# Kernel tuning notes

Hardware: AMD Instinct MI355X
Metric: run time of the kernel (lower is better)

Reference implementation:

```python
import jax, jax.numpy as jnp
import numpy as np

B, S, N, D, H = 4, 2048, 2048, 1024, 16
HD = D // H  # 64
EPS = 1e-5


def layer_norm(x, w, b):
    m = x.mean(axis=-1, keepdims=True)
    v = ((x - m) ** 2).mean(axis=-1, keepdims=True)
    return (x - m) / jnp.sqrt(v + EPS) * w + b


def setup_inputs() -> dict:
    key = jax.random.key(0)
    ks = jax.random.split(key, 4)
    x_q = jax.random.normal(ks[0], (B, S, D), dtype=jnp.float32)
    x_k = jax.random.normal(ks[1], (B, N, HD), dtype=jnp.float32)
    x_v = jax.random.normal(ks[2], (B, N, HD), dtype=jnp.float32)
    # learned params
    qn_w = jnp.ones((HD,), jnp.float32)
    qn_b = jnp.zeros((HD,), jnp.float32)
    kn_w = jnp.ones((HD,), jnp.float32)
    kn_b = jnp.zeros((HD,), jnp.float32)
    n_w = jnp.ones((D,), jnp.float32)
    n_b = jnp.zeros((D,), jnp.float32)
    # xavier-uniform proj weight (D, D), no bias (proj_bias=False)
    limit = np.sqrt(6.0 / (D + D))
    proj_w = jax.random.uniform(ks[3], (D, D), jnp.float32, -limit, limit)
    return {"x_q": x_q, "x_k": x_k, "x_v": x_v,
            "qn_w": qn_w, "qn_b": qn_b, "kn_w": kn_w, "kn_b": kn_b,
            "n_w": n_w, "n_b": n_b, "proj_w": proj_w}


def reference(x_q, x_k, x_v, qn_w, qn_b, kn_w, kn_b, n_w, n_b, proj_w):
    scale = HD ** -0.5
    # faithful to torch: q.reshape(B, H, -1, head_dim) -- NO transpose before reshape
    q = x_q.reshape(B, H, S, HD)
    q = layer_norm(q, qn_w, qn_b)
    k = layer_norm(x_k, kn_w, kn_b)
    q = q * scale
    attn = jnp.einsum('bhsd,bnd->bhsn', q, k)  # (B,H,S,N) shared K across heads
    attn = jax.nn.softmax(attn, axis=-1)
    x = jnp.einsum('bhsn,bnd->bhsd', attn, x_v)  # shared V across heads
    x = jnp.transpose(x, (0, 2, 1, 3)).reshape(B, S, D)
    x = layer_norm(x, n_w, n_b)
    x = x @ proj_w.T  # nn.Linear: x W^T
    return x
```

## Files before the change

kernel.cpp:

```cpp
#include <hip/hip_runtime.h>

#define B_ 4
#define S_ 2048
#define N_ 2048
#define H_ 16
#define D_ 1024

typedef short s4v __attribute__((ext_vector_type(4)));
typedef short s8v __attribute__((ext_vector_type(8)));
typedef float f4v __attribute__((ext_vector_type(4)));
typedef float f2v __attribute__((ext_vector_type(2)));

__device__ __forceinline__ float bf2f(short s) {
  unsigned u = ((unsigned)(unsigned short)s) << 16;
  float f; __builtin_memcpy(&f, &u, 4); return f;
}
__device__ __forceinline__ short f2bf(float f) {
  unsigned u; __builtin_memcpy(&u, &f, 4);
  u += 0x7fffu + ((u >> 16) & 1u);
  return (short)(u >> 16);
}
__device__ __forceinline__ unsigned pack2bf(float a, float b) {
  unsigned ua, ub;
  __builtin_memcpy(&ua, &a, 4);
  __builtin_memcpy(&ub, &b, 4);
  return __builtin_amdgcn_perm(ub + 0x8000u, ua + 0x8000u, 0x07060302u);
}
__device__ __forceinline__ unsigned pk2(float a, float b) {
  unsigned ua, ub;
  __builtin_memcpy(&ua, &a, 4);
  __builtin_memcpy(&ub, &b, 4);
  return __builtin_amdgcn_perm(ub, ua, 0x07060302u);
}
__device__ __forceinline__ s8v load8f32(const float* p) {
  const f4v* q = (const f4v*)p;
  f4v a = q[0], b = q[1];
  union { s8v v; unsigned u[4]; } o;
  o.u[0] = pack2bf(a[0], a[1]); o.u[1] = pack2bf(a[2], a[3]);
  o.u[2] = pack2bf(b[0], b[1]); o.u[3] = pack2bf(b[2], b[3]);
  return o.v;
}
__device__ __forceinline__ void gld16(const char* g, char* l) {
  __builtin_amdgcn_global_load_lds(
      (const __attribute__((address_space(1))) unsigned*)g,
      (__attribute__((address_space(3))) unsigned*)l, 16, 0, 0);
}

__global__ __launch_bounds__(256) void prep_kernel(
    const float* __restrict__ xk, const float* __restrict__ knw,
    const float* __restrict__ knb, short* __restrict__ kws,
    const float* __restrict__ xv, short* __restrict__ vtp,
    const float* __restrict__ pw, const float* __restrict__ nw_,
    const float* __restrict__ nb_, short* __restrict__ wpb,
    float* __restrict__ t12) {
  __shared__ __align__(16) short vstage[4][2048];
  int blk = blockIdx.x;
  if (blk < 2048) {
    int gid = blk * 256 + threadIdx.x;
    int row = gid >> 6, lane = gid & 63;
    float v = xk[(size_t)row * 64 + lane];
    float s = v;
    #pragma unroll
    for (int mm = 1; mm < 64; mm <<= 1) s += __shfl_xor(s, mm, 64);
    float mean = s * 0.015625f;
    float d = v - mean;
    float vs = d * d;
    #pragma unroll
    for (int mm = 1; mm < 64; mm <<= 1) vs += __shfl_xor(vs, mm, 64);
    float rstd = rsqrtf(vs * 0.015625f + 1e-5f);
    kws[(size_t)row * 72 + lane] = f2bf(d * rstd * knw[lane] + knb[lane]);
  } else if (blk < 2112) {
    int wave = threadIdx.x >> 6, lane = threadIdx.x & 63;
    int u = (blk - 2048) * 4 + wave;
    int b = u >> 6, nb = u & 63;
    int r = lane >> 1, dh = lane & 1;
    const float* src = xv + ((size_t)(b * N_ + nb * 32 + r)) * 64 + dh * 32;
    int qq = (r & 15) >> 2;
    int slot = ((r >> 4) << 2) + (r & 3);
    short* wbase = &vstage[wave][0];
    #pragma unroll
    for (int jj = 0; jj < 32; jj += 4) {
      f4v f = *(const f4v*)(src + jj);
      #pragma unroll
      for (int e = 0; e < 4; e++) {
        int d = dh * 32 + jj + e;
        wbase[d * 32 + qq * 8 + slot] = f2bf(f[e]);
      }
    }
    __syncthreads();
    s8v* dst = (s8v*)(vtp + (size_t)u * 2560 + lane * 40);
    const s8v* sp = (const s8v*)(wbase + lane * 32);
    dst[0] = sp[0]; dst[1] = sp[1]; dst[2] = sp[2]; dst[3] = sp[3];
  } else {
    int jr = threadIdx.x >> 4;
    int lc = (threadIdx.x & 15) * 64;
    int j = (blk - 2112) * 16 + jr;
    const float* wr = pw + (size_t)j * 1024 + lc;
    float t1p = 0.f, t2p = 0.f;
    #pragma unroll
    for (int c = 0; c < 64; c += 8) {
      f4v w0 = *(const f4v*)(wr + c);
      f4v w1 = *(const f4v*)(wr + c + 4);
      f4v g0 = *(const f4v*)(nw_ + lc + c);
      f4v g1 = *(const f4v*)(nw_ + lc + c + 4);
      f4v b0 = *(const f4v*)(nb_ + lc + c);
      f4v b1 = *(const f4v*)(nb_ + lc + c + 4);
      float p[8];
      #pragma unroll
      for (int e = 0; e < 4; e++) {
        p[e]     = g0[e] * w0[e];
        p[4 + e] = g1[e] * w1[e];
        t1p += p[e] + p[4 + e];
        t2p += b0[e] * w0[e] + b1[e] * w1[e];
      }
      union { s8v v; unsigned u[4]; } o8;
      o8.u[0] = pack2bf(p[0], p[1]); o8.u[1] = pack2bf(p[2], p[3]);
      o8.u[2] = pack2bf(p[4], p[5]); o8.u[3] = pack2bf(p[6], p[7]);
      *(s8v*)(wpb + (size_t)j * 1024 + lc + c) = o8.v;
    }
    #pragma unroll
    for (int mm = 1; mm < 16; mm <<= 1) {
      t1p += __shfl_xor(t1p, mm, 64);
      t2p += __shfl_xor(t2p, mm, 64);
    }
    if ((threadIdx.x & 15) == 0) { t12[j * 2] = t1p; t12[j * 2 + 1] = t2p; }
  }
}

__global__ __launch_bounds__(256, 4) void flash_kernel(
    const float* __restrict__ xq, const float* __restrict__ qnw,
    const float* __restrict__ qnb, const short* __restrict__ kws,
    const short* __restrict__ vtp, short* __restrict__ aout) {
  __shared__ __align__(16) union {
    char qs[128 * 144];
    struct { char k[2][9216]; char v[2][10240]; } kv;
  } lds;
  int blk = blockIdx.x;
  int sblk = blk & 15, bh = blk >> 4, b = bh >> 4;
  int t = threadIdx.x, wave = t >> 6, lane = t & 63;
  int m = lane & 15, q = lane >> 4;
  const float QSCALE = 0.125f * 1.4426950408889634f;

  const char* kb = (const char*)kws + (size_t)b * N_ * 144;
  const char* vb = (const char*)vtp + (size_t)b * 64 * 5120;

  gld16(vb + t * 16,        lds.kv.v[0] + t * 16);
  gld16(vb + 4096 + t * 16, lds.kv.v[0] + 4096 + t * 16);
  if (t < 128) gld16(vb + 8192 + t * 16, lds.kv.v[0] + 8192 + t * 16);

  {
    int r = t >> 1, half = t & 1;
    const float* qr = xq + ((size_t)bh * S_ + sblk * 128 + r) * 64 + half * 32;
    f4v f[8];
    float s = 0.f, ss = 0.f;
    #pragma unroll
    for (int i = 0; i < 8; i++) {
      f[i] = *(const f4v*)(qr + i * 4);
      s += (f[i][0] + f[i][1]) + (f[i][2] + f[i][3]);
      ss += (f[i][0] * f[i][0] + f[i][1] * f[i][1]) + (f[i][2] * f[i][2] + f[i][3] * f[i][3]);
    }
    s += __shfl_xor(s, 1, 64);
    ss += __shfl_xor(ss, 1, 64);
    float mean = s * 0.015625f;
    float rstd = rsqrtf(ss * 0.015625f - mean * mean + 1e-5f);
    #pragma unroll
    for (int i = 0; i < 4; i++) {
      float y[8];
      #pragma unroll
      for (int e = 0; e < 4; e++) {
        int gi = half * 32 + i * 8;
        y[e]     = ((f[2 * i][e]     - mean) * rstd * qnw[gi + e]     + qnb[gi + e])     * QSCALE;
        y[4 + e] = ((f[2 * i + 1][e] - mean) * rstd * qnw[gi + 4 + e] + qnb[gi + 4 + e]) * QSCALE;
      }
      union { s8v v; unsigned u[4]; } o8;
      #pragma unroll
      for (int e = 0; e < 4; e++) o8.u[e] = pack2bf(y[2 * e], y[2 * e + 1]);
      *(s8v*)(lds.qs + r * 144 + half * 64 + i * 16) = o8.v;
    }
  }
  __syncthreads();

  s8v qlo[2], qhi[2];
  #pragma unroll
  for (int mt = 0; mt < 2; mt++) {
    const char* qrow = lds.qs + (wave * 32 + mt * 16 + m) * 144;
    qlo[mt] = *(const s8v*)(qrow + q * 16);
    qhi[mt] = *(const s8v*)(qrow + 64 + q * 16);
  }
  __syncthreads();

  gld16(kb + t * 16,        lds.kv.k[0] + t * 16);
  gld16(kb + 4096 + t * 16, lds.kv.k[0] + 4096 + t * 16);
  if (t < 64) gld16(kb + 8192 + t * 16, lds.kv.k[0] + 8192 + t * 16);
  __syncthreads();

  f4v zero4 = {0.f, 0.f, 0.f, 0.f};
  f4v o[2][4], lacc[2];
  #pragma unroll
  for (int mt = 0; mt < 2; mt++) {
    lacc[mt] = zero4;
    #pragma unroll
    for (int tt = 0; tt < 4; tt++) o[mt][tt] = zero4;
  }
  s8v ones;
  #pragma unroll
  for (int e = 0; e < 8; e++) ones[e] = (short)0x3F80;

  for (int it = 0; it < 32; ++it) {
    int cur = it & 1;
    if (it < 31) {
      const char* kg = kb + (size_t)(it + 1) * 9216;
      const char* vg = vb + (size_t)(it + 1) * 10240;
      char* kd = lds.kv.k[cur ^ 1];
      char* vd = lds.kv.v[cur ^ 1];
      gld16(kg + t * 16,        kd + t * 16);
      gld16(kg + 4096 + t * 16, kd + 4096 + t * 16);
      if (t < 64) gld16(kg + 8192 + t * 16, kd + 8192 + t * 16);
      gld16(vg + t * 16,        vd + t * 16);
      gld16(vg + 4096 + t * 16, vd + 4096 + t * 16);
      if (t < 128) gld16(vg + 8192 + t * 16, vd + 8192 + t * 16);
    }
    const char* kc = lds.kv.k[cur];
    const char* vc = lds.kv.v[cur];

    #pragma unroll
    for (int g = 0; g < 2; g++) {
      s8v a0lo = *(const s8v*)(kc + (g * 32 + m) * 144 + q * 16);
      s8v a0hi = *(const s8v*)(kc + (g * 32 + m) * 144 + 64 + q * 16);
      s8v a1lo = *(const s8v*)(kc + (g * 32 + 16 + m) * 144 + q * 16);
      s8v a1hi = *(const s8v*)(kc + (g * 32 + 16 + m) * 144 + 64 + q * 16);
      s8v vf[4];
      #pragma unroll
      for (int tt = 0; tt < 4; tt++)
        vf[tt] = *(const s8v*)(vc + g * 5120 + (tt * 16 + m) * 80 + q * 16);

      #pragma unroll
      for (int mt = 0; mt < 2; mt++) {
        f4v s0 = zero4, s1 = zero4;
        s0 = __builtin_amdgcn_mfma_f32_16x16x32_bf16(a0lo, qlo[mt], s0, 0, 0, 0);
        s0 = __builtin_amdgcn_mfma_f32_16x16x32_bf16(a0hi, qhi[mt], s0, 0, 0, 0);
        s1 = __builtin_amdgcn_mfma_f32_16x16x32_bf16(a1lo, qlo[mt], s1, 0, 0, 0);
        s1 = __builtin_amdgcn_mfma_f32_16x16x32_bf16(a1hi, qhi[mt], s1, 0, 0, 0);
        float p[8];
        #pragma unroll
        for (int i = 0; i < 4; i++) {
          p[i]     = __builtin_amdgcn_exp2f(s0[i]);
          p[4 + i] = __builtin_amdgcn_exp2f(s1[i]);
        }
        union { s8v v; unsigned u[4]; } pa;
        #pragma unroll
        for (int i = 0; i < 4; i++) pa.u[i] = pk2(p[2 * i], p[2 * i + 1]);
        lacc[mt] = __builtin_amdgcn_mfma_f32_16x16x32_bf16(pa.v, ones, lacc[mt], 0, 0, 0);
        #pragma unroll
        for (int tt = 0; tt < 4; tt++)
          o[mt][tt] = __builtin_amdgcn_mfma_f32_16x16x32_bf16(pa.v, vf[tt], o[mt][tt], 0, 0, 0);
      }
    }
    __syncthreads();
  }

  #pragma unroll
  for (int mt = 0; mt < 2; mt++) {
    #pragma unroll
    for (int i = 0; i < 4; i++) {
      float inv = __builtin_amdgcn_rcpf(lacc[mt][i]);
      int srow = sblk * 128 + wave * 32 + mt * 16 + q * 4 + i;
      size_t orow = ((size_t)b * S_ + srow) * D_ + (size_t)(bh & 15) * 64;
      #pragma unroll
      for (int tt = 0; tt < 4; tt++)
        aout[orow + tt * 16 + m] = f2bf(o[mt][tt][i] * inv);
    }
  }
}

__global__ __launch_bounds__(256) void ln_d_kernel(
    const short* __restrict__ x, const float* __restrict__ w,
    const float* __restrict__ bb, short* __restrict__ y) {
  int row = blockIdx.x * 4 + (threadIdx.x >> 6);
  int lane = threadIdx.x & 63;
  const short* xr = x + (size_t)row * D_ + lane * 16;
  s8v v0 = *(const s8v*)xr;
  s8v v1 = *(const s8v*)(xr + 8);
  float f[16];
  #pragma unroll
  for (int e = 0; e < 8; e++) { f[e] = bf2f(v0[e]); f[8 + e] = bf2f(v1[e]); }
  float s = 0.f, ss = 0.f;
  #pragma unroll
  for (int e = 0; e < 16; e++) { s += f[e]; ss += f[e] * f[e]; }
  #pragma unroll
  for (int mm = 1; mm < 64; mm <<= 1) {
    s += __shfl_xor(s, mm, 64);
    ss += __shfl_xor(ss, mm, 64);
  }
  float mean = s * (1.0f / 1024.0f);
  float rstd = rsqrtf(ss * (1.0f / 1024.0f) - mean * mean + 1e-5f);
  const float* wp = w + lane * 16;
  const float* bp = bb + lane * 16;
  union { s8v v[2]; short sh[16]; } o;
  #pragma unroll
  for (int e = 0; e < 16; e++)
    o.sh[e] = f2bf((f[e] - mean) * rstd * wp[e] + bp[e]);
  short* yr = y + (size_t)row * D_ + lane * 16;
  *(s8v*)yr = o.v[0];
  *(s8v*)(yr + 8) = o.v[1];
}

__global__ __launch_bounds__(256) void stats_kernel(
    const short* __restrict__ x, float* __restrict__ st) {
  int row = blockIdx.x * 4 + (threadIdx.x >> 6);
  int lane = threadIdx.x & 63;
  const short* xr = x + (size_t)row * D_ + lane * 16;
  s8v v0 = *(const s8v*)xr;
  s8v v1 = *(const s8v*)(xr + 8);
  float s = 0.f, ss = 0.f;
  #pragma unroll
  for (int e = 0; e < 8; e++) {
    float a = bf2f(v0[e]), b = bf2f(v1[e]);
    s += a + b; ss += a * a + b * b;
  }
  #pragma unroll
  for (int mm = 1; mm < 64; mm <<= 1) {
    s += __shfl_xor(s, mm, 64);
    ss += __shfl_xor(ss, mm, 64);
  }
  if (lane == 0) {
    float mean = s * (1.0f / 1024.0f);
    float rstd = rsqrtf(ss * (1.0f / 1024.0f) - mean * mean + 1e-5f);
    f2v o = {rstd, -mean * rstd};
    *(f2v*)(st + (size_t)row * 2) = o;
  }
}

__global__ __launch_bounds__(256, 2) void proj_gemm_fb(
    const short* __restrict__ A, const float* __restrict__ Bw,
    float* __restrict__ C) {
  __shared__ __align__(16) char la[2][16384];
  __shared__ __align__(16) char lb[2][16384];
  int wg = (blockIdx.x & 7) * 64 + (blockIdx.x >> 3);
  int bm = (wg >> 3) * 128;
  int bn = (wg & 7) * 128;
  int t = threadIdx.x, wave = t >> 6, lane = t & 63;
  int m = lane & 15, q = lane >> 4;
  int wm = (wave & 1) * 64, wn = (wave >> 1) * 64;

  int arow0 = t >> 3, au = t & 7;
  const char* abase = (const char*)(A + (size_t)bm * 1024);
  int brow = t >> 1, bu0 = (t & 1) * 4;
  const float* bwbase = Bw + (size_t)(bn + brow) * 1024;
  char* lbrow0 = lb[0] + brow * 128;
  char* lbrow1 = lb[1] + brow * 128;

  f4v zero4 = {0.f, 0.f, 0.f, 0.f};
  f4v acc[4][4];
  #pragma unroll
  for (int i = 0; i < 4; i++)
    #pragma unroll
    for (int j = 0; j < 4; j++) acc[i][j] = zero4;

  #pragma unroll
  for (int c = 0; c < 4; c++) {
    int row = c * 32 + arow0;
    gld16(abase + (size_t)row * 2048 + (size_t)(au ^ (row & 7)) * 16,
          la[0] + c * 4096 + t * 16);
  }
  #pragma unroll
  for (int j = 0; j < 4; j++) {
    int u = bu0 + j;
    s8v bv = load8f32(bwbase + u * 8);
    *(s8v*)(lbrow0 + ((u ^ (brow & 7)) * 16)) = bv;
  }
  __syncthreads();

  for (int it = 0; it < 16; ++it) {
    int cur = it & 1;
    if (it < 15) {
      int k0 = (it + 1) * 64;
      char* ad = la[cur ^ 1];
      char* bd = (cur ^ 1) ? lbrow1 : lbrow0;
      #pragma unroll
      for (int c = 0; c < 4; c++) {
        int row = c * 32 + arow0;
        gld16(abase + (size_t)row * 2048 + (size_t)k0 * 2 +
                  (size_t)(au ^ (row & 7)) * 16,
              ad + c * 4096 + t * 16);
      }
      #pragma unroll
      for (int j = 0; j < 4; j++) {
        int u = bu0 + j;
        s8v bv = load8f32(bwbase + k0 + u * 8);
        *(s8v*)(bd + ((u ^ (brow & 7)) * 16)) = bv;
      }
    }
    const char* lac = la[cur];
    const char* lbc = lb[cur];
    #pragma unroll
    for (int kh = 0; kh < 2; kh++) {
      s8v af[4], bfv[4];
      #pragma unroll
      for (int i = 0; i < 4; i++) {
        int r = wm + i * 16 + m;
        af[i] = *(const s8v*)(lac + r * 128 + (((kh * 4 + q) ^ (r & 7)) * 16));
      }
      #pragma unroll
      for (int j = 0; j < 4; j++) {
        int r = wn + j * 16 + m;
        bfv[j] = *(const s8v*)(lbc + r * 128 + (((kh * 4 + q) ^ (r & 7)) * 16));
      }
      #pragma unroll
      for (int i = 0; i < 4; i++)
        #pragma unroll
        for (int j = 0; j < 4; j++)
          acc[i][j] = __builtin_amdgcn_mfma_f32_16x16x32_bf16(af[i], bfv[j], acc[i][j], 0, 0, 0);
    }
    __syncthreads();
  }

  #pragma unroll
  for (int i = 0; i < 4; i++)
    #pragma unroll
    for (int j = 0; j < 4; j++)
      #pragma unroll
      for (int r = 0; r < 4; r++) {
        int row = bm + wm + i * 16 + q * 4 + r;
        int col = bn + wn + j * 16 + m;
        C[(size_t)row * 1024 + col] = acc[i][j][r];
      }
}

__global__ __launch_bounds__(256, 2) void proj_gemm_fx(
    const short* __restrict__ A, const short* __restrict__ Wp,
    const float* __restrict__ t12, const float* __restrict__ st,
    float* __restrict__ C) {
  __shared__ __align__(16) char la[2][16384];
  __shared__ __align__(16) char lb[2][16384];
  int wg = (blockIdx.x & 7) * 64 + (blockIdx.x >> 3);
  int bm = (wg >> 3) * 128;
  int bn = (wg & 7) * 128;
  int t = threadIdx.x, wave = t >> 6, lane = t & 63;
  int m = lane & 15, q = lane >> 4;
  int wm = (wave & 1) * 64, wn = (wave >> 1) * 64;

  int arow0 = t >> 3, au = t & 7;
  const char* abase = (const char*)(A + (size_t)bm * 1024);
  const char* bbase = (const char*)(Wp + (size_t)bn * 1024);

  f4v zero4 = {0.f, 0.f, 0.f, 0.f};
  f4v acc[4][4];
  #pragma unroll
  for (int i = 0; i < 4; i++)
    #pragma unroll
    for (int j = 0; j < 4; j++) acc[i][j] = zero4;

  #pragma unroll
  for (int c = 0; c < 4; c++) {
    int row = c * 32 + arow0;
    size_t so = (size_t)row * 2048 + (size_t)(au ^ (row & 7)) * 16;
    gld16(abase + so, la[0] + c * 4096 + t * 16);
    gld16(bbase + so, lb[0] + c * 4096 + t * 16);
  }
  __syncthreads();

  for (int it = 0; it < 16; ++it) {
    int cur = it & 1;
    if (it < 15) {
      int k0 = (it + 1) * 64;
      #pragma unroll
      for (int c = 0; c < 4; c++) {
        int row = c * 32 + arow0;
        size_t so = (size_t)row * 2048 + (size_t)k0 * 2 +
                    (size_t)(au ^ (row & 7)) * 16;
        gld16(abase + so, la[cur ^ 1] + c * 4096 + t * 16);
        gld16(bbase + so, lb[cur ^ 1] + c * 4096 + t * 16);
      }
    }
    const char* lac = la[cur];
    const char* lbc = lb[cur];
    #pragma unroll
    for (int kh = 0; kh < 2; kh++) {
      s8v af[4], bfv[4];
      #pragma unroll
      for (int i = 0; i < 4; i++) {
        int r = wm + i * 16 + m;
        af[i] = *(const s8v*)(lac + r * 128 + (((kh * 4 + q) ^ (r & 7)) * 16));
      }
      #pragma unroll
      for (int j = 0; j < 4; j++) {
        int r = wn + j * 16 + m;
        bfv[j] = *(const s8v*)(lbc + r * 128 + (((kh * 4 + q) ^ (r & 7)) * 16));
      }
      #pragma unroll
      for (int i = 0; i < 4; i++)
        #pragma unroll
        for (int j = 0; j < 4; j++)
          acc[i][j] = __builtin_amdgcn_mfma_f32_16x16x32_bf16(af[i], bfv[j], acc[i][j], 0, 0, 0);
    }
    __syncthreads();
  }

  f2v tc[4];
  #pragma unroll
  for (int j = 0; j < 4; j++)
    tc[j] = *(const f2v*)(t12 + (size_t)(bn + wn + j * 16 + m) * 2);
  #pragma unroll
  for (int i = 0; i < 4; i++)
    #pragma unroll
    for (int r = 0; r < 4; r++) {
      int row = bm + wm + i * 16 + q * 4 + r;
      f2v sr_ = *(const f2v*)(st + (size_t)row * 2);
      #pragma unroll
      for (int j = 0; j < 4; j++) {
        int col = bn + wn + j * 16 + m;
        C[(size_t)row * 1024 + col] =
            sr_[0] * acc[i][j][r] + sr_[1] * tc[j][0] + tc[j][1];
      }
    }
}

extern "C" void kernel_launch(void* const* d_in, const int* in_sizes, int n_in,
                              void* d_out, int out_size, void* d_ws, size_t ws_size,
                              hipStream_t stream) {
  const float* xq  = (const float*)d_in[0];
  const float* xk  = (const float*)d_in[1];
  const float* xv  = (const float*)d_in[2];
  const float* qnw = (const float*)d_in[3];
  const float* qnb = (const float*)d_in[4];
  const float* knw = (const float*)d_in[5];
  const float* knb = (const float*)d_in[6];
  const float* nw  = (const float*)d_in[7];
  const float* nb  = (const float*)d_in[8];
  const float* pw  = (const float*)d_in[9];
  float* out = (float*)d_out;

  const size_t NEED = 21438464;
  if (ws_size >= NEED) {
    short* aoutw = (short*)d_ws;
    short* kws = (short*)((char*)d_ws + 16777216);
    short* vtp = (short*)((char*)d_ws + 17956864);
    short* wpb = (short*)((char*)d_ws + 19267584);
    float* t12 = (float*)((char*)d_ws + 21364736);
    float* st  = (float*)((char*)d_ws + 21372928);
    prep_kernel<<<2176, 256, 0, stream>>>(xk, knw, knb, kws, xv, vtp,
                                          pw, nw, nb, wpb, t12);
    flash_kernel<<<1024, 256, 0, stream>>>(xq, qnw, qnb, kws, vtp, aoutw);
    stats_kernel<<<2048, 256, 0, stream>>>(aoutw, st);
    proj_gemm_fx<<<512, 256, 0, stream>>>(aoutw, wpb, t12, st, out);
  } else {
    short* kws = (short*)d_ws;
    short* vtp = (short*)((char*)d_ws + 0x120000);
    short* yws = (short*)d_ws;
    short* aout = (short*)d_out;
    prep_kernel<<<2112, 256, 0, stream>>>(xk, knw, knb, kws, xv, vtp,
                                          pw, nw, nb, (short*)d_ws, (float*)d_ws);
    flash_kernel<<<1024, 256, 0, stream>>>(xq, qnw, qnb, kws, vtp, aout);
    ln_d_kernel<<<B_ * S_ / 4, 256, 0, stream>>>(aout, nw, nb, yws);
    proj_gemm_fb<<<512, 256, 0, stream>>>(yws, pw, out);
  }
}
```

Measured before the change: 201.5 us.

## Fuse output row statistics into flash epilogue via atomics, stagger KV start, set MFMA priority

Removes the separate stats kernel that reread the bf16 attention output. Each flash block now accumulates partial row sums and sums of squares into a zeroed buffer with atomics, and the GEMM epilogue derives mean and rstd from them. The prep kernel gains blocks that zero this buffer. The change also rotates each block's starting KV tile by a batch-dependent offset to spread memory traffic, and raises wave priority around the MFMA sequences. The costs are extra atomic traffic, statistics taken from fp32 values instead of the rounded bf16 output, and a one-pass variance formula.

Result: no change. 202.3 us (+0.4%).

```diff
diff --git a/kernel.cpp b/kernel.cpp
--- a/kernel.cpp
+++ b/kernel.cpp
@@ -52,7 +52,7 @@
     const float* __restrict__ xv, short* __restrict__ vtp,
     const float* __restrict__ pw, const float* __restrict__ nw_,
     const float* __restrict__ nb_, short* __restrict__ wpb,
-    float* __restrict__ t12) {
+    float* __restrict__ t12, float* __restrict__ st) {
   __shared__ __align__(16) short vstage[4][2048];
   int blk = blockIdx.x;
   if (blk < 2048) {
@@ -91,7 +91,7 @@
     s8v* dst = (s8v*)(vtp + (size_t)u * 2560 + lane * 40);
     const s8v* sp = (const s8v*)(wbase + lane * 32);
     dst[0] = sp[0]; dst[1] = sp[1]; dst[2] = sp[2]; dst[3] = sp[3];
-  } else {
+  } else if (blk < 2176) {
     int jr = threadIdx.x >> 4;
     int lc = (threadIdx.x & 15) * 64;
     int j = (blk - 2112) * 16 + jr;
@@ -124,13 +124,19 @@
       t2p += __shfl_xor(t2p, mm, 64);
     }
     if ((threadIdx.x & 15) == 0) { t12[j * 2] = t1p; t12[j * 2 + 1] = t2p; }
+  } else {
+    int idx = (blk - 2176) * 256 + threadIdx.x;
+    f4v z = {0.f, 0.f, 0.f, 0.f};
+    f4v* p = (f4v*)(st + (size_t)idx * 16);
+    p[0] = z; p[1] = z; p[2] = z; p[3] = z;
   }
 }
 
 __global__ __launch_bounds__(256, 4) void flash_kernel(
     const float* __restrict__ xq, const float* __restrict__ qnw,
     const float* __restrict__ qnb, const short* __restrict__ kws,
-    const short* __restrict__ vtp, short* __restrict__ aout) {
+    const short* __restrict__ vtp, short* __restrict__ aout,
+    float* st) {
   __shared__ __align__(16) union {
     char qs[128 * 144];
     struct { char k[2][9216]; char v[2][10240]; } kv;
@@ -140,13 +146,14 @@
   int t = threadIdx.x, wave = t >> 6, lane = t & 63;
   int m = lane & 15, q = lane >> 4;
   const float QSCALE = 0.125f * 1.4426950408889634f;
+  int ofs = ((blk >> 8) & 3) * 8;
 
   const char* kb = (const char*)kws + (size_t)b * N_ * 144;
   const char* vb = (const char*)vtp + (size_t)b * 64 * 5120;
 
-  gld16(vb + t * 16,        lds.kv.v[0] + t * 16);
-  gld16(vb + 4096 + t * 16, lds.kv.v[0] + 4096 + t * 16);
-  if (t < 128) gld16(vb + 8192 + t * 16, lds.kv.v[0] + 8192 + t * 16);
+  gld16(vb + (size_t)ofs * 10240 + t * 16,        lds.kv.v[0] + t * 16);
+  gld16(vb + (size_t)ofs * 10240 + 4096 + t * 16, lds.kv.v[0] + 4096 + t * 16);
+  if (t < 128) gld16(vb + (size_t)ofs * 10240 + 8192 + t * 16, lds.kv.v[0] + 8192 + t * 16);
 
   {
     int r = t >> 1, half = t & 1;
@@ -189,9 +196,9 @@
   }
   __syncthreads();
 
-  gld16(kb + t * 16,        lds.kv.k[0] + t * 16);
-  gld16(kb + 4096 + t * 16, lds.kv.k[0] + 4096 + t * 16);
-  if (t < 64) gld16(kb + 8192 + t * 16, lds.kv.k[0] + 8192 + t * 16);
+  gld16(kb + (size_t)ofs * 9216 + t * 16,        lds.kv.k[0] + t * 16);
+  gld16(kb + (size_t)ofs * 9216 + 4096 + t * 16, lds.kv.k[0] + 4096 + t * 16);
+  if (t < 64) gld16(kb + (size_t)ofs * 9216 + 8192 + t * 16, lds.kv.k[0] + 8192 + t * 16);
   __syncthreads();
 
   f4v zero4 = {0.f, 0.f, 0.f, 0.f};
@@ -209,8 +216,9 @@
   for (int it = 0; it < 32; ++it) {
     int cur = it & 1;
     if (it < 31) {
-      const char* kg = kb + (size_t)(it + 1) * 9216;
-      const char* vg = vb + (size_t)(it + 1) * 10240;
+      int td1 = (it + 1 + ofs) & 31;
+      const char* kg = kb + (size_t)td1 * 9216;
+      const char* vg = vb + (size_t)td1 * 10240;
       char* kd = lds.kv.k[cur ^ 1];
       char* vd = lds.kv.v[cur ^ 1];
       gld16(kg + t * 16,        kd + t * 16);
@@ -237,10 +245,12 @@
       #pragma unroll
       for (int mt = 0; mt < 2; mt++) {
         f4v s0 = zero4, s1 = zero4;
+        __builtin_amdgcn_s_setprio(1);
         s0 = __builtin_amdgcn_mfma_f32_16x16x32_bf16(a0lo, qlo[mt], s0, 0, 0, 0);
         s0 = __builtin_amdgcn_mfma_f32_16x16x32_bf16(a0hi, qhi[mt], s0, 0, 0, 0);
         s1 = __builtin_amdgcn_mfma_f32_16x16x32_bf16(a1lo, qlo[mt], s1, 0, 0, 0);
         s1 = __builtin_amdgcn_mfma_f32_16x16x32_bf16(a1hi, qhi[mt], s1, 0, 0, 0);
+        __builtin_amdgcn_s_setprio(0);
         float p[8];
         #pragma unroll
         for (int i = 0; i < 4; i++) {
@@ -250,10 +260,12 @@
         union { s8v v; unsigned u[4]; } pa;
         #pragma unroll
         for (int i = 0; i < 4; i++) pa.u[i] = pk2(p[2 * i], p[2 * i + 1]);
+        __builtin_amdgcn_s_setprio(1);
         lacc[mt] = __builtin_amdgcn_mfma_f32_16x16x32_bf16(pa.v, ones, lacc[mt], 0, 0, 0);
         #pragma unroll
         for (int tt = 0; tt < 4; tt++)
           o[mt][tt] = __builtin_amdgcn_mfma_f32_16x16x32_bf16(pa.v, vf[tt], o[mt][tt], 0, 0, 0);
+        __builtin_amdgcn_s_setprio(0);
       }
     }
     __syncthreads();
@@ -266,9 +278,23 @@
       float inv = __builtin_amdgcn_rcpf(lacc[mt][i]);
       int srow = sblk * 128 + wave * 32 + mt * 16 + q * 4 + i;
       size_t orow = ((size_t)b * S_ + srow) * D_ + (size_t)(bh & 15) * 64;
-      #pragma unroll
-      for (int tt = 0; tt < 4; tt++)
-        aout[orow + tt * 16 + m] = f2bf(o[mt][tt][i] * inv);
+      float ps = 0.f, pss = 0.f;
+      #pragma unroll
+      for (int tt = 0; tt < 4; tt++) {
+        float v = o[mt][tt][i] * inv;
+        ps += v; pss += v * v;
+        aout[orow + tt * 16 + m] = f2bf(v);
+      }
+      #pragma unroll
+      for (int mm = 1; mm < 16; mm <<= 1) {
+        ps += __shfl_xor(ps, mm, 64);
+        pss += __shfl_xor(pss, mm, 64);
+      }
+      if (m == 0) {
+        size_t gr = (size_t)b * S_ + srow;
+        atomicAdd(&st[gr * 2], ps);
+        atomicAdd(&st[gr * 2 + 1], pss);
+      }
     }
   }
 }
@@ -303,32 +329,6 @@
   short* yr = y + (size_t)row * D_ + lane * 16;
   *(s8v*)yr = o.v[0];
   *(s8v*)(yr + 8) = o.v[1];
-}
-
-__global__ __launch_bounds__(256) void stats_kernel(
-    const short* __restrict__ x, float* __restrict__ st) {
-  int row = blockIdx.x * 4 + (threadIdx.x >> 6);
-  int lane = threadIdx.x & 63;
-  const short* xr = x + (size_t)row * D_ + lane * 16;
-  s8v v0 = *(const s8v*)xr;
-  s8v v1 = *(const s8v*)(xr + 8);
-  float s = 0.f, ss = 0.f;
-  #pragma unroll
-  for (int e = 0; e < 8; e++) {
-    float a = bf2f(v0[e]), b = bf2f(v1[e]);
-    s += a + b; ss += a * a + b * b;
-  }
-  #pragma unroll
-  for (int mm = 1; mm < 64; mm <<= 1) {
-    s += __shfl_xor(s, mm, 64);
-    ss += __shfl_xor(ss, mm, 64);
-  }
-  if (lane == 0) {
-    float mean = s * (1.0f / 1024.0f);
-    float rstd = rsqrtf(ss * (1.0f / 1024.0f) - mean * mean + 1e-5f);
-    f2v o = {rstd, -mean * rstd};
-    *(f2v*)(st + (size_t)row * 2) = o;
-  }
 }
 
 __global__ __launch_bounds__(256, 2) void proj_gemm_fb(
@@ -507,11 +507,14 @@
     for (int r = 0; r < 4; r++) {
       int row = bm + wm + i * 16 + q * 4 + r;
       f2v sr_ = *(const f2v*)(st + (size_t)row * 2);
+      float mean = sr_[0] * (1.0f / 1024.0f);
+      float rstd = rsqrtf(sr_[1] * (1.0f / 1024.0f) - mean * mean + 1e-5f);
+      float mrs = -mean * rstd;
       #pragma unroll
       for (int j = 0; j < 4; j++) {
         int col = bn + wn + j * 16 + m;
         C[(size_t)row * 1024 + col] =
-            sr_[0] * acc[i][j][r] + sr_[1] * tc[j][0] + tc[j][1];
+            rstd * acc[i][j][r] + mrs * tc[j][0] + tc[j][1];
       }
     }
 }
@@ -539,19 +542,20 @@
     short* wpb = (short*)((char*)d_ws + 19267584);
     float* t12 = (float*)((char*)d_ws + 21364736);
     float* st  = (float*)((char*)d_ws + 21372928);
-    prep_kernel<<<2176, 256, 0, stream>>>(xk, knw, knb, kws, xv, vtp,
-                                          pw, nw, nb, wpb, t12);
-    flash_kernel<<<1024, 256, 0, stream>>>(xq, qnw, qnb, kws, vtp, aoutw);
-    stats_kernel<<<2048, 256, 0, stream>>>(aoutw, st);
+    prep_kernel<<<2180, 256, 0, stream>>>(xk, knw, knb, kws, xv, vtp,
+                                          pw, nw, nb, wpb, t12, st);
+    flash_kernel<<<1024, 256, 0, stream>>>(xq, qnw, qnb, kws, vtp, aoutw, st);
     proj_gemm_fx<<<512, 256, 0, stream>>>(aoutw, wpb, t12, st, out);
   } else {
     short* kws = (short*)d_ws;
     short* vtp = (short*)((char*)d_ws + 0x120000);
     short* yws = (short*)d_ws;
     short* aout = (short*)d_out;
+    float* stdummy = (float*)((char*)d_ws + 0x220000);
     prep_kernel<<<2112, 256, 0, stream>>>(xk, knw, knb, kws, xv, vtp,
-                                          pw, nw, nb, (short*)d_ws, (float*)d_ws);
-    flash_kernel<<<1024, 256, 0, stream>>>(xq, qnw, qnb, kws, vtp, aout);
+                                          pw, nw, nb, (short*)d_ws, (float*)d_ws,
+                                          stdummy);
+    flash_kernel<<<1024, 256, 0, stream>>>(xq, qnw, qnb, kws, vtp, aout, stdummy);
     ln_d_kernel<<<B_ * S_ / 4, 256, 0, stream>>>(aout, nw, nb, yws);
     proj_gemm_fb<<<512, 256, 0, stream>>>(yws, pw, out);
   }
```
